# Kernel optimization log

Measured on AMD Instinct MI355X. Metric: run time of the kernel, lower is better.

## Reference

```python
import jax, jax.numpy as jnp
import numpy as np

N_TRAJ, T, D_DATA, D_LAT, N_UNITS = 8192, 100, 32, 64, 100

def setup_inputs() -> dict:
    key = jax.random.key(0)
    ks = jax.random.split(key, 12)
    w = lambda k, *shape: jax.random.normal(k, shape, jnp.float32) * 0.05
    z = lambda n: jnp.zeros((n,), jnp.float32)
    return {
        "data": jax.random.normal(ks[0], (N_TRAJ, T, D_DATA), jnp.float32),
        "time_steps": jnp.linspace(0.0, 1.0, T, dtype=jnp.float32),  # uniform grid -> dt < interval/50 always
        "prior": jax.random.normal(ks[1], (N_TRAJ, D_LAT), jnp.float32),
        # ODE func MLP: latent -> n_units -> latent
        "Wo1": w(ks[2], D_LAT, N_UNITS), "bo1": z(N_UNITS),
        "Wo2": w(ks[3], N_UNITS, D_LAT), "bo2": z(D_LAT),
        # GRU update/reset/candidate gates, each a 2-layer MLP on concat(y, x)
        "Wz1": w(ks[4], D_LAT + D_DATA, N_UNITS), "bz1": z(N_UNITS),
        "Wz2": w(ks[5], N_UNITS, D_LAT), "bz2": z(D_LAT),
        "Wr1": w(ks[6], D_LAT + D_DATA, N_UNITS), "br1": z(N_UNITS),
        "Wr2": w(ks[7], N_UNITS, D_LAT), "br2": z(D_LAT),
        "Wh1": w(ks[8], D_LAT + D_DATA, N_UNITS), "bh1": z(N_UNITS),
        "Wh2": w(ks[9], N_UNITS, D_LAT), "bh2": z(D_LAT),
    }

def _odernn(data, time_steps, prior,
            Wo1, bo1, Wo2, bo2,
            Wz1, bz1, Wz2, bz2,
            Wr1, br1, Wr2, br2,
            Wh1, bh1, Wh2, bh2):
    # Replicates the original loop's (prev_t, t_i) bookkeeping faithfully:
    # iteration 1 uses dt = ts[1] - ts[0]; after each iteration the code sets
    # prev_t, t_i = ts[i], ts[i-1], so iteration i >= 2 uses dt = ts[i-2] - ts[i-1].
    dts = jnp.concatenate([time_steps[1:2] - time_steps[0:1],
                           time_steps[:-2] - time_steps[1:-1]])  # [T-1]
    xs = jnp.swapaxes(data[:, 1:, :], 0, 1)  # [T-1, N, D_DATA] for scan

    def ode_func(y):  # [N, D_LAT] -> [N, D_LAT]
        return jnp.tanh(y @ Wo1 + bo1) @ Wo2 + bo2

    def gru_update(y, x):  # [N, D_LAT], [N, D_DATA] -> [N, D_LAT]
        yx = jnp.concatenate([y, x], axis=-1)
        zg = jax.nn.sigmoid(jnp.tanh(yx @ Wz1 + bz1) @ Wz2 + bz2)
        rg = jax.nn.sigmoid(jnp.tanh(yx @ Wr1 + br1) @ Wr2 + br2)
        ryx = jnp.concatenate([rg * y, x], axis=-1)
        h = jnp.tanh(jnp.tanh(ryx @ Wh1 + bh1) @ Wh2 + bh2)
        return (1.0 - zg) * h + zg * y

    def step(y, inp):
        dt, x = inp
        # |dt| < minimum_step branch: single explicit-Euler increment
        y_ode = y + ode_func(y) * dt
        return gru_update(y_ode, x), None

    y_final, _ = jax.lax.scan(step, prior, (dts, xs))
    return y_final

def reference(data, time_steps, prior,
              Wo1, bo1, Wo2, bo2,
              Wz1, bz1, Wz2, bz2,
              Wr1, br1, Wr2, br2,
              Wh1, bh1, Wh2, bh2):
    return _odernn(data, time_steps, prior,
                   Wo1, bo1, Wo2, bo2,
                   Wz1, bz1, Wz2, bz2,
                   Wr1, br1, Wr2, br2,
                   Wh1, bh1, Wh2, bh2)
```

## Files before the change

### kernel.cpp

```cpp
#include <hip/hip_runtime.h>

#define T_STEPS 100
#define NTRAJ   8192
#define MBLK    32
#define W_TILES 112
#define W_BYTES (W_TILES * 1024)
#define TILEBUF 18432
#define LDS_TOTAL (W_BYTES + 2 * TILEBUF)

typedef __attribute__((ext_vector_type(8))) _Float16 f16x8;
typedef __attribute__((ext_vector_type(4))) _Float16 f16x4;
typedef __attribute__((ext_vector_type(2))) __fp16   h16x2;
typedef __attribute__((ext_vector_type(4))) float    f32x4;

#define MFMA16(a, b, c) __builtin_amdgcn_mfma_f32_16x16x32_f16((a), (b), (c), 0, 0, 0)

#define SWZ(row, col) ((col) ^ (((row) & 7) << 3))

__device__ __forceinline__ float fast_tanh(float x) {
    float e = __expf(2.f * x);
    return 1.f - 2.f * __builtin_amdgcn_rcpf(1.f + e);
}
__device__ __forceinline__ float fast_sigmoid(float x) {
    float e = __expf(-x);
    return __builtin_amdgcn_rcpf(1.f + e);
}

__global__ void pack_kernel(const float* __restrict__ Wo1, const float* __restrict__ Wo2,
                            const float* __restrict__ Wz1, const float* __restrict__ Wz2,
                            const float* __restrict__ Wr1, const float* __restrict__ Wr2,
                            const float* __restrict__ Wh1, const float* __restrict__ Wh2,
                            _Float16* __restrict__ P)
{
    int idx = blockIdx.x * 256 + threadIdx.x;
    if (idx >= 144 * 512) return;
    int tile = idx >> 9;
    int r    = idx & 511;
    int lane = r >> 3, j = r & 7;
    int krel = ((lane >> 4) << 3) + j;
    int c16  = lane & 15;
    float val = 0.f;

    if (tile < 14) {
        int t = tile, nt = t >> 1, kt = t & 1;
        int k = kt * 32 + krel, n = nt * 16 + c16;
        if (k < 64 && n < 100) val = Wo1[k * 100 + n];
    } else if (tile < 30) {
        int t = tile - 14, nt = t >> 2, kt = t & 3;
        int k = kt * 32 + krel, n = nt * 16 + c16;
        if (k < 100) val = Wo2[k * 64 + n];
    } else if (tile < 75) {
        int t = tile - 30, nt = t / 3, kt = t % 3;
        int k = kt * 32 + krel;
        if (nt < 7)      { int n = nt * 16 + c16;        if (n < 100) val = Wz1[k * 100 + n]; }
        else if (nt >= 8){ int n = (nt - 8) * 16 + c16;  if (n < 100) val = Wr1[k * 100 + n]; }
    } else if (tile < 107) {
        int t = tile - 75, gate = t >> 4, rem = t & 15, nt = rem >> 2, kt = rem & 3;
        int k = kt * 32 + krel, n = nt * 16 + c16;
        const float* W = gate ? Wr2 : Wz2;
        if (k < 100) val = W[k * 64 + n];
    } else if (tile < 128) {
        int t = tile - 107, nt = t / 3, kt = t % 3;
        int k = kt * 32 + krel, n = nt * 16 + c16;
        if (n < 100) val = Wh1[k * 100 + n];
    } else {
        int t = tile - 128, nt = t >> 2, kt = t & 3;
        int k = kt * 32 + krel, n = nt * 16 + c16;
        if (k < 100) val = Wh2[k * 64 + n];
    }
    P[idx] = (_Float16)val;
}

__device__ __forceinline__ f16x8 ldsA(const _Float16* buf, int stride, int row, int kcol) {
    return *(const f16x8*)(buf + row * stride + SWZ(row, kcol));
}
__device__ __forceinline__ void st4(_Float16* buf, int stride, int traj, int f0,
                                    float a, float b, float c, float d) {
    f16x4 h = {(_Float16)a, (_Float16)b, (_Float16)c, (_Float16)d};
    *(f16x4*)(buf + traj * stride + SWZ(traj, f0)) = h;
}
__device__ __forceinline__ f32x4 loadBias4(const float* b, int f0, int n) {
    f32x4 v = {0.f, 0.f, 0.f, 0.f};
    #pragma unroll
    for (int r = 0; r < 4; ++r) if (f0 + r < n) v[r] = b[f0 + r];
    return v;
}
__device__ __forceinline__ f16x8 cvt8(f32x4 a, f32x4 b) {
    union { h16x2 h2[4]; f16x8 v; } u;
    u.h2[0] = __builtin_amdgcn_cvt_pkrtz(a[0], a[1]);
    u.h2[1] = __builtin_amdgcn_cvt_pkrtz(a[2], a[3]);
    u.h2[2] = __builtin_amdgcn_cvt_pkrtz(b[0], b[1]);
    u.h2[3] = __builtin_amdgcn_cvt_pkrtz(b[2], b[3]);
    return u.v;
}

__global__ __launch_bounds__(512, 2) void odernn_kernel(
    const float* __restrict__ data, const float* __restrict__ ts,
    const float* __restrict__ prior,
    const float* __restrict__ bo1, const float* __restrict__ bo2,
    const float* __restrict__ bz1, const float* __restrict__ bz2,
    const float* __restrict__ br1, const float* __restrict__ br2,
    const float* __restrict__ bh1, const float* __restrict__ bh2,
    const _Float16* __restrict__ P, float* __restrict__ out)
{
    extern __shared__ __align__(16) char smem[];
    _Float16* W = (_Float16*)smem;

    const int tid  = threadIdx.x;
    const int lane = tid & 63;
    const int wv   = tid >> 6;
    const int tg   = wv >> 2;
    const int wq   = wv & 3;
    const int c16  = lane & 15;
    const int g4   = lane >> 4;
    const int m0   = blockIdx.x * MBLK + tg * 16;
    const int f0   = wq * 16 + (g4 << 2);
    const f16x8* Pt = (const f16x8*)P;
    const f16x8* Wv = (const f16x8*)W;

    _Float16* base = (_Float16*)(smem + W_BYTES + tg * TILEBUF);
    _Float16* sYb = base;
    _Float16* sYX = base + 1024;
    _Float16* sRX = base + 2048;
    _Float16* sH1 = base + 3072;
    _Float16* sZR = base + 5120;

    {
        f16x8* Wd = (f16x8*)W;
        #pragma unroll
        for (int it = 0; it < 14; ++it) {
            int idx = tid + it * 512;
            int ldst = idx >> 6, l = idx & 63;
            int srct = (ldst < 14) ? ldst : ldst + 16;
            Wd[idx] = Pt[srct * 64 + l];
        }
    }

    f32x4 bo1v[2], bh1v[2], bzrv[4];
    #pragma unroll
    for (int t = 0; t < 2; ++t) {
        int nt = wq + 4 * t;
        f32x4 zo = {0.f,0.f,0.f,0.f};
        if (nt < 7) {
            int ft = nt * 16 + (g4 << 2);
            bo1v[t] = loadBias4(bo1, ft, 100);
            bh1v[t] = loadBias4(bh1, ft, 100);
        } else { bo1v[t] = zo; bh1v[t] = zo; }
    }
    #pragma unroll
    for (int q = 0; q < 4; ++q) {
        int i = wq + 4 * q;
        f32x4 v = {0.f,0.f,0.f,0.f};
        if (i < 14) {
            int bt = (i < 7) ? i : i + 1;
            int ft = bt * 16 + (g4 << 2);
            if (i < 7) v = loadBias4(bz1, ft, 100);
            else       v = loadBias4(br1, ft - 128, 100);
        }
        bzrv[q] = v;
    }
    const f32x4 bo2v = *(const f32x4*)(bo2 + f0);
    const f32x4 bz2v = *(const f32x4*)(bz2 + f0);
    const f32x4 br2v = *(const f32x4*)(br2 + f0);
    const f32x4 bh2v = *(const f32x4*)(bh2 + f0);

    f16x8 Ao2[4], Ah2[4];
    #pragma unroll
    for (int kt = 0; kt < 4; ++kt) {
        Ao2[kt] = Pt[(14 + wq * 4 + kt) * 64 + lane];
        Ah2[kt] = Pt[(128 + wq * 4 + kt) * 64 + lane];
    }

    float y[4], yo[4] = {0,0,0,0}, zg[4] = {0,0,0,0};
    {
        f32x4 pv = *(const f32x4*)(prior + (size_t)(m0 + c16) * 64 + f0);
        #pragma unroll
        for (int r = 0; r < 4; ++r) y[r] = pv[r];
        st4(sYb, 64, c16, f0, y[0], y[1], y[2], y[3]);
    }
    {
        int row32 = tid >> 4, col = 112 + (tid & 15);
        int t = row32 >> 4, r16 = row32 & 15;
        _Float16* h1 = (_Float16*)(smem + W_BYTES + t * TILEBUF) + 3072;
        h1[r16 * 128 + SWZ(r16, col)] = (_Float16)0.f;
    }
    for (int i = tid; i < 2 * 16 * 32; i += 512) {
        int t = i >> 9, rem = i & 511;
        int r16 = rem >> 5, cc = rem & 31;
        int col = (cc < 16) ? (112 + cc) : (224 + cc);
        _Float16* zr = (_Float16*)(smem + W_BYTES + t * TILEBUF) + 5120;
        zr[r16 * 256 + SWZ(r16, col)] = (_Float16)0.f;
    }
    __syncthreads();

    const float t0v = ts[0], t1v = ts[1];

    const float* xptr = data + (size_t)(m0 + c16) * (T_STEPS * 32) + 32 + (g4 << 3);
    f32x4 xn0 = *(const f32x4*)(xptr);
    f32x4 xn1 = *(const f32x4*)(xptr + 4);
    f16x8 xfrag = cvt8(xn0, xn1);

    #pragma unroll 1
    for (int s = 0; s < T_STEPS - 1; ++s) {
        const float dt = (s == 0) ? (t1v - t0v) : (ts[s - 1] - ts[s]);

        xptr += 32;
        if (s < T_STEPS - 2) {
            xn0 = *(const f32x4*)(xptr);
            xn1 = *(const f32x4*)(xptr + 4);
        }
        f32x4 xacc3[4];
        {
            f16x8 b0 = ldsA(sYb, 64, c16, (g4 << 3));
            f16x8 b1 = ldsA(sYb, 64, c16, 32 + (g4 << 3));
            #pragma unroll
            for (int t = 0; t < 2; ++t) {
                int nt = wq + 4 * t;
                if (nt < 7) {
                    f32x4 acc0 = bo1v[t];
                    f32x4 z4 = {0.f, 0.f, 0.f, 0.f};
                    acc0 = MFMA16(Wv[(nt * 2 + 0) * 64 + lane], b0, acc0);
                    f32x4 acc1 = MFMA16(Wv[(nt * 2 + 1) * 64 + lane], b1, z4);
                    int ft = nt * 16 + (g4 << 2);
                    st4(sH1, 128, c16, ft,
                        fast_tanh(acc0[0] + acc1[0]), fast_tanh(acc0[1] + acc1[1]),
                        fast_tanh(acc0[2] + acc1[2]), fast_tanh(acc0[3] + acc1[3]));
                }
            }
            #pragma unroll
            for (int q = 0; q < 4; ++q) {
                int i = wq + 4 * q;
                if (i < 14) {
                    int bt = (i < 7) ? i : i + 1;
                    xacc3[q] = MFMA16(Wv[(14 + bt * 3 + 2) * 64 + lane], xfrag, bzrv[q]);
                }
            }
        }
        __syncthreads();

        f32x4 xacc5[2];
        {
            f32x4 acc0 = bo2v;
            f32x4 z4 = {0.f, 0.f, 0.f, 0.f};
            acc0 = MFMA16(Ao2[0], ldsA(sH1, 128, c16, 0 * 32 + (g4 << 3)), acc0);
            f32x4 acc1 = MFMA16(Ao2[1], ldsA(sH1, 128, c16, 1 * 32 + (g4 << 3)), z4);
            acc0 = MFMA16(Ao2[2], ldsA(sH1, 128, c16, 2 * 32 + (g4 << 3)), acc0);
            acc1 = MFMA16(Ao2[3], ldsA(sH1, 128, c16, 3 * 32 + (g4 << 3)), acc1);
            #pragma unroll
            for (int t = 0; t < 2; ++t) {
                int nt = wq + 4 * t;
                if (nt < 7)
                    xacc5[t] = MFMA16(Wv[(91 + nt * 3 + 2) * 64 + lane], xfrag, bh1v[t]);
            }
            #pragma unroll
            for (int r = 0; r < 4; ++r) yo[r] = y[r] + dt * (acc0[r] + acc1[r]);
            st4(sYX, 64, c16, f0, yo[0], yo[1], yo[2], yo[3]);
        }
        __syncthreads();

        {
            f16x8 b0 = ldsA(sYX, 64, c16, (g4 << 3));
            f16x8 b1 = ldsA(sYX, 64, c16, 32 + (g4 << 3));
            #pragma unroll
            for (int q = 0; q < 4; ++q) {
                int i = wq + 4 * q;
                if (i < 14) {
                    int bt = (i < 7) ? i : i + 1;
                    f32x4 acc = MFMA16(Wv[(14 + bt * 3 + 0) * 64 + lane], b0, xacc3[q]);
                    acc = MFMA16(Wv[(14 + bt * 3 + 1) * 64 + lane], b1, acc);
                    int ft = bt * 16 + (g4 << 2);
                    st4(sZR, 256, c16, ft,
                        fast_tanh(acc[0]), fast_tanh(acc[1]),
                        fast_tanh(acc[2]), fast_tanh(acc[3]));
                }
            }
        }
        __syncthreads();

        {
            f32x4 accz0 = bz2v, accr0 = br2v;
            f32x4 z4 = {0.f, 0.f, 0.f, 0.f};
            f32x4 accz1 = z4, accr1 = z4;
            accz0 = MFMA16(Wv[(59 + wq * 4 + 0) * 64 + lane], ldsA(sZR, 256, c16, 0 * 32 + (g4 << 3)), accz0);
            accr0 = MFMA16(Wv[(75 + wq * 4 + 0) * 64 + lane], ldsA(sZR, 256, c16, 128 + 0 * 32 + (g4 << 3)), accr0);
            accz1 = MFMA16(Wv[(59 + wq * 4 + 1) * 64 + lane], ldsA(sZR, 256, c16, 1 * 32 + (g4 << 3)), accz1);
            accr1 = MFMA16(Wv[(75 + wq * 4 + 1) * 64 + lane], ldsA(sZR, 256, c16, 128 + 1 * 32 + (g4 << 3)), accr1);
            accz0 = MFMA16(Wv[(59 + wq * 4 + 2) * 64 + lane], ldsA(sZR, 256, c16, 2 * 32 + (g4 << 3)), accz0);
            accr0 = MFMA16(Wv[(75 + wq * 4 + 2) * 64 + lane], ldsA(sZR, 256, c16, 128 + 2 * 32 + (g4 << 3)), accr0);
            accz1 = MFMA16(Wv[(59 + wq * 4 + 3) * 64 + lane], ldsA(sZR, 256, c16, 3 * 32 + (g4 << 3)), accz1);
            accr1 = MFMA16(Wv[(75 + wq * 4 + 3) * 64 + lane], ldsA(sZR, 256, c16, 128 + 3 * 32 + (g4 << 3)), accr1);
            float rv[4];
            #pragma unroll
            for (int r = 0; r < 4; ++r) {
                zg[r] = fast_sigmoid(accz0[r] + accz1[r]);
                rv[r] = fast_sigmoid(accr0[r] + accr1[r]) * yo[r];
            }
            st4(sRX, 64, c16, f0, rv[0], rv[1], rv[2], rv[3]);
        }
        __syncthreads();

        {
            f16x8 b0 = ldsA(sRX, 64, c16, (g4 << 3));
            f16x8 b1 = ldsA(sRX, 64, c16, 32 + (g4 << 3));
            #pragma unroll
            for (int t = 0; t < 2; ++t) {
                int nt = wq + 4 * t;
                if (nt < 7) {
                    f32x4 acc = MFMA16(Wv[(91 + nt * 3 + 0) * 64 + lane], b0, xacc5[t]);
                    acc = MFMA16(Wv[(91 + nt * 3 + 1) * 64 + lane], b1, acc);
                    int ft = nt * 16 + (g4 << 2);
                    st4(sH1, 128, c16, ft,
                        fast_tanh(acc[0]), fast_tanh(acc[1]),
                        fast_tanh(acc[2]), fast_tanh(acc[3]));
                }
            }
        }
        __syncthreads();

        {
            f32x4 acc0 = bh2v;
            f32x4 z4 = {0.f, 0.f, 0.f, 0.f};
            acc0 = MFMA16(Ah2[0], ldsA(sH1, 128, c16, 0 * 32 + (g4 << 3)), acc0);
            f32x4 acc1 = MFMA16(Ah2[1], ldsA(sH1, 128, c16, 1 * 32 + (g4 << 3)), z4);
            acc0 = MFMA16(Ah2[2], ldsA(sH1, 128, c16, 2 * 32 + (g4 << 3)), acc0);
            acc1 = MFMA16(Ah2[3], ldsA(sH1, 128, c16, 3 * 32 + (g4 << 3)), acc1);
            #pragma unroll
            for (int r = 0; r < 4; ++r) {
                float h = fast_tanh(acc0[r] + acc1[r]);
                y[r] = (1.f - zg[r]) * h + zg[r] * yo[r];
            }
            st4(sYb, 64, c16, f0, y[0], y[1], y[2], y[3]);
        }
        __syncthreads();

        xfrag = cvt8(xn0, xn1);
    }

    {
        f32x4 ov = {y[0], y[1], y[2], y[3]};
        *(f32x4*)(out + (size_t)(m0 + c16) * 64 + f0) = ov;
    }
}

extern "C" void kernel_launch(void* const* d_in, const int* in_sizes, int n_in,
                              void* d_out, int out_size, void* d_ws, size_t ws_size,
                              hipStream_t stream) {
    const float* data = (const float*)d_in[0];
    const float* ts   = (const float*)d_in[1];
    const float* prior= (const float*)d_in[2];
    const float* Wo1 = (const float*)d_in[3];  const float* bo1 = (const float*)d_in[4];
    const float* Wo2 = (const float*)d_in[5];  const float* bo2 = (const float*)d_in[6];
    const float* Wz1 = (const float*)d_in[7];  const float* bz1 = (const float*)d_in[8];
    const float* Wz2 = (const float*)d_in[9];  const float* bz2 = (const float*)d_in[10];
    const float* Wr1 = (const float*)d_in[11]; const float* br1 = (const float*)d_in[12];
    const float* Wr2 = (const float*)d_in[13]; const float* br2 = (const float*)d_in[14];
    const float* Wh1 = (const float*)d_in[15]; const float* bh1 = (const float*)d_in[16];
    const float* Wh2 = (const float*)d_in[17]; const float* bh2 = (const float*)d_in[18];
    _Float16* P = (_Float16*)d_ws;
    float* out = (float*)d_out;

    (void)hipFuncSetAttribute((const void*)odernn_kernel,
                              hipFuncAttributeMaxDynamicSharedMemorySize, LDS_TOTAL);

    hipLaunchKernelGGL(pack_kernel, dim3((144 * 512 + 255) / 256), dim3(256), 0, stream,
                       Wo1, Wo2, Wz1, Wz2, Wr1, Wr2, Wh1, Wh2, P);
    hipLaunchKernelGGL(odernn_kernel, dim3(NTRAJ / MBLK), dim3(512), LDS_TOTAL, stream,
                       data, ts, prior, bo1, bo2, bz1, bz2, br1, br2, bh1, bh2, P, out);
}
```

Baseline: 298.9 us.

## Hold all MLP weight fragments in registers instead of LDS

Each wave now loads its MFMA weight fragments for every gate layer from the packed global buffer into registers once, before the time loop. The 112 KB LDS weight region and the dynamic-LDS attribute call are removed, leaving only the per-group activation tiles in LDS. The goal is to remove repeated LDS weight reads inside the recurrent loop and to let more blocks share a CU. In exchange, about 38 f16x8 fragments stay live per thread under a 512x2 launch bound, which risks register spills. It also adds a barrier that waits only on lgkmcnt, so the global prefetches of x can stay in flight across barriers, and switches tanh/sigmoid to exp2f with prescaled constants.

```diff
diff --git a/kernel.cpp b/kernel.cpp
--- a/kernel.cpp
+++ b/kernel.cpp
@@ -3,10 +3,8 @@
 #define T_STEPS 100
 #define NTRAJ   8192
 #define MBLK    32
-#define W_TILES 112
-#define W_BYTES (W_TILES * 1024)
 #define TILEBUF 18432
-#define LDS_TOTAL (W_BYTES + 2 * TILEBUF)
+#define LDS_TOTAL (2 * TILEBUF)
 
 typedef __attribute__((ext_vector_type(8))) _Float16 f16x8;
 typedef __attribute__((ext_vector_type(4))) _Float16 f16x4;
@@ -17,12 +15,18 @@
 
 #define SWZ(row, col) ((col) ^ (((row) & 7) << 3))
 
+#define BAR() do { \
+    asm volatile("s_waitcnt lgkmcnt(0)" ::: "memory"); \
+    __builtin_amdgcn_s_barrier(); \
+    asm volatile("" ::: "memory"); \
+} while (0)
+
 __device__ __forceinline__ float fast_tanh(float x) {
-    float e = __expf(2.f * x);
+    float e = exp2f(x * 2.885390081777927f);
     return 1.f - 2.f * __builtin_amdgcn_rcpf(1.f + e);
 }
 __device__ __forceinline__ float fast_sigmoid(float x) {
-    float e = __expf(-x);
+    float e = exp2f(x * -1.4426950408889634f);
     return __builtin_amdgcn_rcpf(1.f + e);
 }
 
@@ -104,7 +108,6 @@
     const _Float16* __restrict__ P, float* __restrict__ out)
 {
     extern __shared__ __align__(16) char smem[];
-    _Float16* W = (_Float16*)smem;
 
     const int tid  = threadIdx.x;
     const int lane = tid & 63;
@@ -116,24 +119,45 @@
     const int m0   = blockIdx.x * MBLK + tg * 16;
     const int f0   = wq * 16 + (g4 << 2);
     const f16x8* Pt = (const f16x8*)P;
-    const f16x8* Wv = (const f16x8*)W;
-
-    _Float16* base = (_Float16*)(smem + W_BYTES + tg * TILEBUF);
+
+    _Float16* base = (_Float16*)(smem + tg * TILEBUF);
     _Float16* sYb = base;
     _Float16* sYX = base + 1024;
     _Float16* sRX = base + 2048;
     _Float16* sH1 = base + 3072;
     _Float16* sZR = base + 5120;
 
-    {
-        f16x8* Wd = (f16x8*)W;
-        #pragma unroll
-        for (int it = 0; it < 14; ++it) {
-            int idx = tid + it * 512;
-            int ldst = idx >> 6, l = idx & 63;
-            int srct = (ldst < 14) ? ldst : ldst + 16;
-            Wd[idx] = Pt[srct * 64 + l];
-        }
+    int bt3[4];
+    #pragma unroll
+    for (int q = 0; q < 4; ++q) {
+        int i = wq + 4 * q;
+        bt3[q] = (i < 14) ? ((i < 7) ? i : i + 1) : 0;
+    }
+    const int nt1a = wq, nt1b = (wq + 4 < 7) ? wq + 4 : 6;
+
+    f16x8 Wg1[2][2], Wg3[4][2], Wx3[4], Wg4z[4], Wg4r[4], Wg5[2][2], Wx5[2];
+    f16x8 Ao2[4], Ah2[4];
+    #pragma unroll
+    for (int kt = 0; kt < 2; ++kt) {
+        Wg1[0][kt] = Pt[(nt1a * 2 + kt) * 64 + lane];
+        Wg1[1][kt] = Pt[(nt1b * 2 + kt) * 64 + lane];
+        Wg5[0][kt] = Pt[(107 + nt1a * 3 + kt) * 64 + lane];
+        Wg5[1][kt] = Pt[(107 + nt1b * 3 + kt) * 64 + lane];
+    }
+    Wx5[0] = Pt[(107 + nt1a * 3 + 2) * 64 + lane];
+    Wx5[1] = Pt[(107 + nt1b * 3 + 2) * 64 + lane];
+    #pragma unroll
+    for (int q = 0; q < 4; ++q) {
+        Wg3[q][0] = Pt[(30 + bt3[q] * 3 + 0) * 64 + lane];
+        Wg3[q][1] = Pt[(30 + bt3[q] * 3 + 1) * 64 + lane];
+        Wx3[q]    = Pt[(30 + bt3[q] * 3 + 2) * 64 + lane];
+    }
+    #pragma unroll
+    for (int kt = 0; kt < 4; ++kt) {
+        Wg4z[kt] = Pt[(75 + wq * 4 + kt) * 64 + lane];
+        Wg4r[kt] = Pt[(91 + wq * 4 + kt) * 64 + lane];
+        Ao2[kt]  = Pt[(14 + wq * 4 + kt) * 64 + lane];
+        Ah2[kt]  = Pt[(128 + wq * 4 + kt) * 64 + lane];
     }
 
     f32x4 bo1v[2], bh1v[2], bzrv[4];
@@ -152,7 +176,7 @@
         int i = wq + 4 * q;
         f32x4 v = {0.f,0.f,0.f,0.f};
         if (i < 14) {
-            int bt = (i < 7) ? i : i + 1;
+            int bt = bt3[q];
             int ft = bt * 16 + (g4 << 2);
             if (i < 7) v = loadBias4(bz1, ft, 100);
             else       v = loadBias4(br1, ft - 128, 100);
@@ -163,13 +187,6 @@
     const f32x4 bz2v = *(const f32x4*)(bz2 + f0);
     const f32x4 br2v = *(const f32x4*)(br2 + f0);
     const f32x4 bh2v = *(const f32x4*)(bh2 + f0);
-
-    f16x8 Ao2[4], Ah2[4];
-    #pragma unroll
-    for (int kt = 0; kt < 4; ++kt) {
-        Ao2[kt] = Pt[(14 + wq * 4 + kt) * 64 + lane];
-        Ah2[kt] = Pt[(128 + wq * 4 + kt) * 64 + lane];
-    }
 
     float y[4], yo[4] = {0,0,0,0}, zg[4] = {0,0,0,0};
     {
@@ -181,14 +198,14 @@
     {
         int row32 = tid >> 4, col = 112 + (tid & 15);
         int t = row32 >> 4, r16 = row32 & 15;
-        _Float16* h1 = (_Float16*)(smem + W_BYTES + t * TILEBUF) + 3072;
+        _Float16* h1 = (_Float16*)(smem + t * TILEBUF) + 3072;
         h1[r16 * 128 + SWZ(r16, col)] = (_Float16)0.f;
     }
     for (int i = tid; i < 2 * 16 * 32; i += 512) {
         int t = i >> 9, rem = i & 511;
         int r16 = rem >> 5, cc = rem & 31;
         int col = (cc < 16) ? (112 + cc) : (224 + cc);
-        _Float16* zr = (_Float16*)(smem + W_BYTES + t * TILEBUF) + 5120;
+        _Float16* zr = (_Float16*)(smem + t * TILEBUF) + 5120;
         zr[r16 * 256 + SWZ(r16, col)] = (_Float16)0.f;
     }
     __syncthreads();
@@ -219,8 +236,8 @@
                 if (nt < 7) {
                     f32x4 acc0 = bo1v[t];
                     f32x4 z4 = {0.f, 0.f, 0.f, 0.f};
-                    acc0 = MFMA16(Wv[(nt * 2 + 0) * 64 + lane], b0, acc0);
-                    f32x4 acc1 = MFMA16(Wv[(nt * 2 + 1) * 64 + lane], b1, z4);
+                    acc0 = MFMA16(Wg1[t][0], b0, acc0);
+                    f32x4 acc1 = MFMA16(Wg1[t][1], b1, z4);
                     int ft = nt * 16 + (g4 << 2);
                     st4(sH1, 128, c16, ft,
                         fast_tanh(acc0[0] + acc1[0]), fast_tanh(acc0[1] + acc1[1]),
@@ -230,13 +247,10 @@
             #pragma unroll
             for (int q = 0; q < 4; ++q) {
                 int i = wq + 4 * q;
-                if (i < 14) {
-                    int bt = (i < 7) ? i : i + 1;
-                    xacc3[q] = MFMA16(Wv[(14 + bt * 3 + 2) * 64 + lane], xfrag, bzrv[q]);
-                }
-            }
-        }
-        __syncthreads();
+                if (i < 14) xacc3[q] = MFMA16(Wx3[q], xfrag, bzrv[q]);
+            }
+        }
+        BAR();
 
         f32x4 xacc5[2];
         {
@@ -249,14 +263,13 @@
             #pragma unroll
             for (int t = 0; t < 2; ++t) {
                 int nt = wq + 4 * t;
-                if (nt < 7)
-                    xacc5[t] = MFMA16(Wv[(91 + nt * 3 + 2) * 64 + lane], xfrag, bh1v[t]);
+                if (nt < 7) xacc5[t] = MFMA16(Wx5[t], xfrag, bh1v[t]);
             }
             #pragma unroll
             for (int r = 0; r < 4; ++r) yo[r] = y[r] + dt * (acc0[r] + acc1[r]);
             st4(sYX, 64, c16, f0, yo[0], yo[1], yo[2], yo[3]);
         }
-        __syncthreads();
+        BAR();
 
         {
             f16x8 b0 = ldsA(sYX, 64, c16, (g4 << 3));
@@ -265,30 +278,29 @@
             for (int q = 0; q < 4; ++q) {
                 int i = wq + 4 * q;
                 if (i < 14) {
-                    int bt = (i < 7) ? i : i + 1;
-                    f32x4 acc = MFMA16(Wv[(14 + bt * 3 + 0) * 64 + lane], b0, xacc3[q]);
-                    acc = MFMA16(Wv[(14 + bt * 3 + 1) * 64 + lane], b1, acc);
-                    int ft = bt * 16 + (g4 << 2);
+                    f32x4 acc = MFMA16(Wg3[q][0], b0, xacc3[q]);
+                    acc = MFMA16(Wg3[q][1], b1, acc);
+                    int ft = bt3[q] * 16 + (g4 << 2);
                     st4(sZR, 256, c16, ft,
                         fast_tanh(acc[0]), fast_tanh(acc[1]),
                         fast_tanh(acc[2]), fast_tanh(acc[3]));
                 }
             }
         }
-        __syncthreads();
+        BAR();
 
         {
             f32x4 accz0 = bz2v, accr0 = br2v;
             f32x4 z4 = {0.f, 0.f, 0.f, 0.f};
             f32x4 accz1 = z4, accr1 = z4;
-            accz0 = MFMA16(Wv[(59 + wq * 4 + 0) * 64 + lane], ldsA(sZR, 256, c16, 0 * 32 + (g4 << 3)), accz0);
-            accr0 = MFMA16(Wv[(75 + wq * 4 + 0) * 64 + lane], ldsA(sZR, 256, c16, 128 + 0 * 32 + (g4 << 3)), accr0);
-            accz1 = MFMA16(Wv[(59 + wq * 4 + 1) * 64 + lane], ldsA(sZR, 256, c16, 1 * 32 + (g4 << 3)), accz1);
-            accr1 = MFMA16(Wv[(75 + wq * 4 + 1) * 64 + lane], ldsA(sZR, 256, c16, 128 + 1 * 32 + (g4 << 3)), accr1);
-            accz0 = MFMA16(Wv[(59 + wq * 4 + 2) * 64 + lane], ldsA(sZR, 256, c16, 2 * 32 + (g4 << 3)), accz0);
-            accr0 = MFMA16(Wv[(75 + wq * 4 + 2) * 64 + lane], ldsA(sZR, 256, c16, 128 + 2 * 32 + (g4 << 3)), accr0);
-            accz1 = MFMA16(Wv[(59 + wq * 4 + 3) * 64 + lane], ldsA(sZR, 256, c16, 3 * 32 + (g4 << 3)), accz1);
-            accr1 = MFMA16(Wv[(75 + wq * 4 + 3) * 64 + lane], ldsA(sZR, 256, c16, 128 + 3 * 32 + (g4 << 3)), accr1);
+            accz0 = MFMA16(Wg4z[0], ldsA(sZR, 256, c16, 0 * 32 + (g4 << 3)), accz0);
+            accr0 = MFMA16(Wg4r[0], ldsA(sZR, 256, c16, 128 + 0 * 32 + (g4 << 3)), accr0);
+            accz1 = MFMA16(Wg4z[1], ldsA(sZR, 256, c16, 1 * 32 + (g4 << 3)), accz1);
+            accr1 = MFMA16(Wg4r[1], ldsA(sZR, 256, c16, 128 + 1 * 32 + (g4 << 3)), accr1);
+            accz0 = MFMA16(Wg4z[2], ldsA(sZR, 256, c16, 2 * 32 + (g4 << 3)), accz0);
+            accr0 = MFMA16(Wg4r[2], ldsA(sZR, 256, c16, 128 + 2 * 32 + (g4 << 3)), accr0);
+            accz1 = MFMA16(Wg4z[3], ldsA(sZR, 256, c16, 3 * 32 + (g4 << 3)), accz1);
+            accr1 = MFMA16(Wg4r[3], ldsA(sZR, 256, c16, 128 + 3 * 32 + (g4 << 3)), accr1);
             float rv[4];
             #pragma unroll
             for (int r = 0; r < 4; ++r) {
@@ -297,7 +309,7 @@
             }
             st4(sRX, 64, c16, f0, rv[0], rv[1], rv[2], rv[3]);
         }
-        __syncthreads();
+        BAR();
 
         {
             f16x8 b0 = ldsA(sRX, 64, c16, (g4 << 3));
@@ -306,8 +318,8 @@
             for (int t = 0; t < 2; ++t) {
                 int nt = wq + 4 * t;
                 if (nt < 7) {
-                    f32x4 acc = MFMA16(Wv[(91 + nt * 3 + 0) * 64 + lane], b0, xacc5[t]);
-                    acc = MFMA16(Wv[(91 + nt * 3 + 1) * 64 + lane], b1, acc);
+                    f32x4 acc = MFMA16(Wg5[t][0], b0, xacc5[t]);
+                    acc = MFMA16(Wg5[t][1], b1, acc);
                     int ft = nt * 16 + (g4 << 2);
                     st4(sH1, 128, c16, ft,
                         fast_tanh(acc[0]), fast_tanh(acc[1]),
@@ -315,7 +327,7 @@
                 }
             }
         }
-        __syncthreads();
+        BAR();
 
         {
             f32x4 acc0 = bh2v;
@@ -331,7 +343,7 @@
             }
             st4(sYb, 64, c16, f0, y[0], y[1], y[2], y[3]);
         }
-        __syncthreads();
+        BAR();
 
         xfrag = cvt8(xn0, xn1);
     }
@@ -359,9 +371,6 @@
     _Float16* P = (_Float16*)d_ws;
     float* out = (float*)d_out;
 
-    (void)hipFuncSetAttribute((const void*)odernn_kernel,
-                              hipFuncAttributeMaxDynamicSharedMemorySize, LDS_TOTAL);
-
     hipLaunchKernelGGL(pack_kernel, dim3((144 * 512 + 255) / 256), dim3(256), 0, stream,
                        Wo1, Wo2, Wz1, Wz2, Wr1, Wr2, Wh1, Wh2, P);
     hipLaunchKernelGGL(odernn_kernel, dim3(NTRAJ / MBLK), dim3(512), LDS_TOTAL, stream,
```

After: 447.0 us. 49.6% more time.
